# Kernel tuning notes

Hardware: AMD Instinct MI355X
Metric: run time of the kernel (lower is better)

Reference implementation:

```python
import jax, jax.numpy as jnp
import numpy as np
from jax import lax

BETA = 0.1

def setup_inputs() -> dict:
    key = jax.random.key(0)
    k = jax.random.split(key, 6)
    B, T, H, V = 2, 1024, 1024, 64000
    return {
        "_input": jax.random.normal(k[0], (B, T, H), jnp.float32) * 0.02,
        "weight": jax.random.normal(k[1], (V, H), jnp.float32) * 0.02,
        "attention_mask": (jax.random.uniform(k[2], (B, T)) < 0.9).astype(jnp.float32),
        "rewards": jax.random.normal(k[3], (B,), jnp.float32),
        "ref_input": jax.random.normal(k[4], (B, T, H), jnp.float32) * 0.02,
        "ref_weight": jax.random.normal(k[5], (V, H), jnp.float32) * 0.02,
    }


def _grpo(log_probs, attention_mask, rewards, ref_log_probs, beta):
    # log_probs: [B,T,V]
    chosen = jnp.argmax(log_probs, axis=-1)  # [B,T] int
    tok_lp = jnp.take_along_axis(log_probs, chosen[..., None], axis=-1)[..., 0]  # [B,T]
    ref_tok_lp = lax.stop_gradient(
        jnp.take_along_axis(ref_log_probs, chosen[..., None], axis=-1)[..., 0]
    )
    adv = (rewards - rewards.mean()) / (jnp.std(rewards, ddof=1) + 1e-8)  # [B]
    ratio = jnp.exp(tok_lp - lax.stop_gradient(tok_lp))  # == 1 in fwd, grad-carrying
    policy_loss = -ratio * adv[:, None]
    d = ref_tok_lp - tok_lp
    kl = jnp.exp(d) - d - 1.0
    per_tok = (policy_loss + beta * kl) * attention_mask
    seqlen = jnp.clip(attention_mask.sum(axis=1), 1.0)
    loss = (per_tok.sum(axis=1) / seqlen).mean()
    metrics = (
        tok_lp.mean(),
        jnp.std(tok_lp, ddof=1),
        log_probs.mean(),
        (kl * attention_mask).sum(axis=1).mean() / attention_mask.sum(axis=1).mean(),
    )
    return loss, metrics


def reference(_input, weight, attention_mask, rewards, ref_input, ref_weight):
    logits = jnp.einsum("bth,vh->btv", _input, weight)
    log_probs = jax.nn.log_softmax(logits, axis=-1)
    ref_logits = jnp.einsum("bth,vh->btv", ref_input, ref_weight)
    ref_log_probs = lax.stop_gradient(jax.nn.log_softmax(ref_logits, axis=-1))
    loss, metrics = _grpo(log_probs, attention_mask, rewards, ref_log_probs, BETA)
    return (loss, *metrics)
```

## Files before the change

### kernel.cpp

```cpp
#include <hip/hip_runtime.h>
#include <math.h>

#define GRPO_BETA 0.1f

constexpr int BM = 128;
constexpr int BN = 256;
constexpr int BK = 32;

typedef __attribute__((ext_vector_type(4))) float   f32x4;
typedef __attribute__((ext_vector_type(8))) __bf16  bf16x8;

__device__ __forceinline__ float sexp_fast(float a) { return __expf(fminf(a, 0.f)); }
__device__ __forceinline__ float sexp(float a)      { return expf(fminf(a, 0.f)); }

__device__ __forceinline__ bf16x8 cvt8(float4 a, float4 b) {
  bf16x8 r;
  r[0] = (__bf16)a.x; r[1] = (__bf16)a.y; r[2] = (__bf16)a.z; r[3] = (__bf16)a.w;
  r[4] = (__bf16)b.x; r[5] = (__bf16)b.y; r[6] = (__bf16)b.z; r[7] = (__bf16)b.w;
  return r;
}

__device__ __forceinline__ void bar_lgkm() {
  asm volatile("s_waitcnt lgkmcnt(0)\n\ts_barrier" ::: "memory");
}

__global__ __launch_bounds__(256)
void cvt_bf16_kernel(const float* __restrict__ src, __bf16* __restrict__ dst,
                     long long n8)
{
  long long i = (long long)blockIdx.x * blockDim.x + threadIdx.x;
  const long long stride = (long long)gridDim.x * blockDim.x;
  for (; i < n8; i += stride) {
    const float4 a = *reinterpret_cast<const float4*>(src + i * 8);
    const float4 b = *reinterpret_cast<const float4*>(src + i * 8 + 4);
    *reinterpret_cast<bf16x8*>(dst + i * 8) = cvt8(a, b);
  }
}

template <bool CVT, bool FULL>
__global__ __launch_bounds__(512, 4)
void fused_gemm_reduce(const float* __restrict__ AfP, const float* __restrict__ WfP,
                       const float* __restrict__ AfR, const float* __restrict__ WfR,
                       const __bf16* __restrict__ AhP, const __bf16* __restrict__ WhP,
                       const __bf16* __restrict__ AhR, const __bf16* __restrict__ WhR,
                       float* __restrict__ partP, float* __restrict__ partR,
                       int M, int K, int V, int NC, int NL, int gx)
{
  __shared__ __align__(16) unsigned short lds_a[BM * 64];
  __shared__ __align__(16) unsigned short lds_w[BN * 64];
  __shared__ __align__(16) float4 lds_red[BM * 4];

  const int tid  = threadIdx.x;
  const int lane = tid & 63;
  const int wave = tid >> 6;
  const int wm   = wave >> 2;
  const int wn   = wave & 3;
  const int l15  = lane & 15;
  const int q    = lane >> 4;

  const int nb  = gridDim.x;
  int wl = blockIdx.x;
  if ((nb & 7) == 0) wl = (wl & 7) * (nb >> 3) + (wl >> 3);
  const bool isPol = (wl & 1) == 0;
  const int  w2    = wl >> 1;
  const int  bx    = w2 % gx;
  const int  chunk = w2 / gx;
  const int  row0  = bx * BM;

  const float*  Af = isPol ? AfP : AfR;
  const float*  Wf = isPol ? WfP : WfR;
  const __bf16* Ah = isPol ? AhP : AhR;
  const __bf16* Wh = isPol ? WhP : WhR;

  const int t3 = tid & 3;
  const int r4 = tid >> 2;
  const int stw = ((t3 * 16) ^ ((r4 & 7) << 4));
  const int sta = r4 * 128 + stw;

  const int arow = min(row0 + r4, M - 1);
  const int aro  = arow * K + t3 * 8;

  const int swzr  = ((q * 16) ^ ((l15 & 7) << 4));
  const int aoff0 = (wm * 64 + l15) * 128 + swzr;
  const int woff0 = (wn * 64 + l15) * 128 + swzr;

  float rm = -INFINITY, rse = 0.f, rsum = 0.f;
  int   ridx = 0x7fffffff;

  const int NS = K / BK;

  for (int sub = 0; sub < NL; ++sub) {
    const int v0 = (chunk * NL + sub) * BN;
    if (v0 >= V) break;

    int wro[2];
#pragma unroll
    for (int i = 0; i < 2; ++i)
      wro[i] = min(v0 + r4 + 128 * i, V - 1) * K + t3 * 8;

    f32x4 acc[4][4];
#pragma unroll
    for (int i = 0; i < 4; ++i)
#pragma unroll
      for (int j = 0; j < 4; ++j) acc[i][j] = (f32x4){0.f, 0.f, 0.f, 0.f};

    float4 aF[2], wF[2][2];
    bf16x8 aH, wH[2];

    if constexpr (CVT) {
      aF[0] = *reinterpret_cast<const float4*>(Af + aro);
      aF[1] = *reinterpret_cast<const float4*>(Af + aro + 4);
#pragma unroll
      for (int i = 0; i < 2; ++i) {
        wF[i][0] = *reinterpret_cast<const float4*>(Wf + wro[i]);
        wF[i][1] = *reinterpret_cast<const float4*>(Wf + wro[i] + 4);
      }
      *reinterpret_cast<bf16x8*>(reinterpret_cast<char*>(lds_a) + sta) = cvt8(aF[0], aF[1]);
#pragma unroll
      for (int i = 0; i < 2; ++i)
        *reinterpret_cast<bf16x8*>(reinterpret_cast<char*>(lds_w) + (r4 + 128 * i) * 128 + stw) =
            cvt8(wF[i][0], wF[i][1]);
      if (NS > 1) {
        aF[0] = *reinterpret_cast<const float4*>(Af + aro + BK);
        aF[1] = *reinterpret_cast<const float4*>(Af + aro + BK + 4);
#pragma unroll
        for (int i = 0; i < 2; ++i) {
          wF[i][0] = *reinterpret_cast<const float4*>(Wf + wro[i] + BK);
          wF[i][1] = *reinterpret_cast<const float4*>(Wf + wro[i] + BK + 4);
        }
      }
    } else {
      aH = *reinterpret_cast<const bf16x8*>(Ah + aro);
#pragma unroll
      for (int i = 0; i < 2; ++i)
        wH[i] = *reinterpret_cast<const bf16x8*>(Wh + wro[i]);
      *reinterpret_cast<bf16x8*>(reinterpret_cast<char*>(lds_a) + sta) = aH;
#pragma unroll
      for (int i = 0; i < 2; ++i)
        *reinterpret_cast<bf16x8*>(reinterpret_cast<char*>(lds_w) + (r4 + 128 * i) * 128 + stw) = wH[i];
      if (NS > 1) {
        aH = *reinterpret_cast<const bf16x8*>(Ah + aro + BK);
#pragma unroll
        for (int i = 0; i < 2; ++i)
          wH[i] = *reinterpret_cast<const bf16x8*>(Wh + wro[i] + BK);
      }
    }
    bar_lgkm();

    for (int s = 0; s < NS; ++s) {
      const int p = (s & 1) << 6;

      bf16x8 afr[4];
#pragma unroll
      for (int f = 0; f < 4; ++f)
        afr[f] = *reinterpret_cast<const bf16x8*>(
            reinterpret_cast<const char*>(lds_a) + (aoff0 ^ p) + f * 2048);
      __builtin_amdgcn_s_setprio(1);
#pragma unroll
      for (int fn = 0; fn < 4; ++fn) {
        bf16x8 wfr = *reinterpret_cast<const bf16x8*>(
            reinterpret_cast<const char*>(lds_w) + (woff0 ^ p) + fn * 2048);
#pragma unroll
        for (int fm = 0; fm < 4; ++fm)
          acc[fm][fn] = __builtin_amdgcn_mfma_f32_16x16x32_bf16(
              afr[fm], wfr, acc[fm][fn], 0, 0, 0);
      }
      __builtin_amdgcn_s_setprio(0);

      if (s + 1 < NS) {
        const int p1 = ((s + 1) & 1) << 6;
        if constexpr (CVT) {
          *reinterpret_cast<bf16x8*>(reinterpret_cast<char*>(lds_a) + (sta ^ p1)) =
              cvt8(aF[0], aF[1]);
#pragma unroll
          for (int i = 0; i < 2; ++i)
            *reinterpret_cast<bf16x8*>(
                reinterpret_cast<char*>(lds_w) + (((r4 + 128 * i) * 128 + stw) ^ p1)) =
                cvt8(wF[i][0], wF[i][1]);
          if (s + 2 < NS) {
            const int kf = (s + 2) * BK;
            aF[0] = *reinterpret_cast<const float4*>(Af + aro + kf);
            aF[1] = *reinterpret_cast<const float4*>(Af + aro + kf + 4);
#pragma unroll
            for (int i = 0; i < 2; ++i) {
              wF[i][0] = *reinterpret_cast<const float4*>(Wf + wro[i] + kf);
              wF[i][1] = *reinterpret_cast<const float4*>(Wf + wro[i] + kf + 4);
            }
          }
        } else {
          *reinterpret_cast<bf16x8*>(reinterpret_cast<char*>(lds_a) + (sta ^ p1)) = aH;
#pragma unroll
          for (int i = 0; i < 2; ++i)
            *reinterpret_cast<bf16x8*>(
                reinterpret_cast<char*>(lds_w) + (((r4 + 128 * i) * 128 + stw) ^ p1)) = wH[i];
          if (s + 2 < NS) {
            const int kf = (s + 2) * BK;
            aH = *reinterpret_cast<const bf16x8*>(Ah + aro + kf);
#pragma unroll
            for (int i = 0; i < 2; ++i)
              wH[i] = *reinterpret_cast<const bf16x8*>(Wh + wro[i] + kf);
          }
        }
      }
      bar_lgkm();
    }

#pragma unroll
    for (int fm = 0; fm < 4; ++fm) {
#pragma unroll
      for (int reg = 0; reg < 4; ++reg) {
        float lm = -INFINITY;
#pragma unroll
        for (int fn = 0; fn < 4; ++fn) {
          if (FULL || v0 + wn * 64 + fn * 16 + l15 < V)
            lm = fmaxf(lm, acc[fm][fn][reg]);
        }
#pragma unroll
        for (int d = 1; d < 16; d <<= 1) lm = fmaxf(lm, __shfl_xor(lm, d));
        float se = 0.f, sm = 0.f; int li = 0x7fffffff;
#pragma unroll
        for (int fn = 0; fn < 4; ++fn) {
          const int v = v0 + wn * 64 + fn * 16 + l15;
          if (FULL || v < V) {
            const float x = acc[fm][fn][reg];
            se += __expf(x - lm);
            if (isPol) {
              sm += x;
              if (x == lm) li = min(li, v);
            }
          }
        }
        if (isPol) {
#pragma unroll
          for (int d = 1; d < 16; d <<= 1) {
            se += __shfl_xor(se, d);
            sm += __shfl_xor(sm, d);
            li  = min(li, __shfl_xor(li, d));
          }
        } else {
#pragma unroll
          for (int d = 1; d < 16; d <<= 1) se += __shfl_xor(se, d);
        }
        if (l15 == 0) {
          const int row = wm * 64 + fm * 16 + q * 4 + reg;
          lds_red[row * 4 + wn] = make_float4(lm, se, sm, __int_as_float(li));
        }
      }
    }
    __syncthreads();

    if (tid < BM) {
      float4 p0 = lds_red[tid * 4];
      float m = p0.x, se = p0.y, sm = p0.z; int idx = __float_as_int(p0.w);
#pragma unroll
      for (int j = 1; j < 4; ++j) {
        const float4 t = lds_red[tid * 4 + j];
        const int ti = __float_as_int(t.w);
        const float nm = fmaxf(m, t.x);
        se = se * sexp_fast(m - nm) + t.y * sexp_fast(t.x - nm);
        if (isPol) {
          sm += t.z;
          if (t.x > m || (t.x == m && ti < idx)) idx = ti;
        }
        m = nm;
      }
      const float nm = fmaxf(rm, m);
      rse = rse * sexp_fast(rm - nm) + se * sexp_fast(m - nm);
      if (isPol) {
        rsum += sm;
        if (m > rm || (m == rm && idx < ridx)) ridx = idx;
      }
      rm = nm;
    }
    __syncthreads();
  }

  if (tid < BM) {
    const int row = row0 + tid;
    if (row < M) {
      if (isPol) {
        reinterpret_cast<float4*>(partP)[(size_t)row * NC + chunk] =
            make_float4(rm, rse, rsum, __int_as_float(ridx));
      } else {
        reinterpret_cast<float2*>(partR)[(size_t)row * NC + chunk] =
            make_float2(rm, rse);
      }
    }
  }
}

__global__ __launch_bounds__(256)
void combine_kernel(const float4* __restrict__ partP,
                    const float2* __restrict__ partR,
                    const float* __restrict__ refA,
                    const float* __restrict__ refW,
                    float4* __restrict__ rowtab,
                    int M, int K, int V, int NC)
{
  const int row = blockIdx.x;
  const int tid = threadIdx.x;

  __shared__ float redf[256];
  __shared__ int   redi[256];
  __shared__ float s_M, s_SE, s_SUM, s_Mr, s_SEr, s_dot;
  __shared__ int   s_idx;

  float m = -INFINITY, se = 0.f, sm = 0.f; int idx = 0x7fffffff;
  for (int i = tid; i < NC; i += 256) {
    float4 p = partP[(size_t)row * NC + i];
    int pi = __float_as_int(p.w);
    float nm = fmaxf(m, p.x);
    se = se * sexp(m - nm) + p.y * sexp(p.x - nm);
    if (p.x > m || (p.x == m && pi < idx)) idx = pi;
    m = nm;
    sm += p.z;
  }
  redf[tid] = m; redi[tid] = idx;
  __syncthreads();
  for (int s = 128; s > 0; s >>= 1) {
    if (tid < s) {
      float om = redf[tid + s]; int oi = redi[tid + s];
      if (om > redf[tid] || (om == redf[tid] && oi < redi[tid])) { redf[tid] = om; redi[tid] = oi; }
    }
    __syncthreads();
  }
  if (tid == 0) { s_M = redf[0]; s_idx = redi[0]; }
  __syncthreads();
  const float Mp = s_M; const int chosen = s_idx;

  float contrib = se * sexp(m - Mp);
  __syncthreads();
  redf[tid] = contrib; __syncthreads();
  for (int s = 128; s > 0; s >>= 1) { if (tid < s) redf[tid] += redf[tid + s]; __syncthreads(); }
  if (tid == 0) s_SE = redf[0];
  __syncthreads();
  redf[tid] = sm; __syncthreads();
  for (int s = 128; s > 0; s >>= 1) { if (tid < s) redf[tid] += redf[tid + s]; __syncthreads(); }
  if (tid == 0) s_SUM = redf[0];
  __syncthreads();

  float mr = -INFINITY, ser = 0.f;
  for (int i = tid; i < NC; i += 256) {
    float2 p = partR[(size_t)row * NC + i];
    float nm = fmaxf(mr, p.x);
    ser = ser * sexp(mr - nm) + p.y * sexp(p.x - nm);
    mr = nm;
  }
  redf[tid] = mr; __syncthreads();
  for (int s = 128; s > 0; s >>= 1) { if (tid < s) redf[tid] = fmaxf(redf[tid], redf[tid + s]); __syncthreads(); }
  if (tid == 0) s_Mr = redf[0];
  __syncthreads();
  const float Mr = s_Mr;
  float contribr = ser * sexp(mr - Mr);
  __syncthreads();
  redf[tid] = contribr; __syncthreads();
  for (int s = 128; s > 0; s >>= 1) { if (tid < s) redf[tid] += redf[tid + s]; __syncthreads(); }
  if (tid == 0) s_SEr = redf[0];
  __syncthreads();

  float dp = 0.f;
  const float* ar = refA + (size_t)row * K;
  const float* wr = refW + (size_t)chosen * K;
  for (int j = tid * 4; j < K; j += 256 * 4) {
    float4 x = *reinterpret_cast<const float4*>(ar + j);
    float4 y = *reinterpret_cast<const float4*>(wr + j);
    dp = fmaf(x.x, y.x, dp);
    dp = fmaf(x.y, y.y, dp);
    dp = fmaf(x.z, y.z, dp);
    dp = fmaf(x.w, y.w, dp);
  }
  __syncthreads();
  redf[tid] = dp; __syncthreads();
  for (int s = 128; s > 0; s >>= 1) { if (tid < s) redf[tid] += redf[tid + s]; __syncthreads(); }
  if (tid == 0) s_dot = redf[0];
  __syncthreads();

  if (tid == 0) {
    float lse     = Mp + logf(s_SE);
    float tok     = Mp - lse;
    float ref_lse = Mr + logf(s_SEr);
    float ref_tok = s_dot - ref_lse;
    float d  = ref_tok - tok;
    float kl = expm1f(d) - d;
    float rm3 = s_SUM / (float)V - lse;
    rowtab[row] = make_float4(tok, kl, rm3, 0.f);
  }
}

__global__ __launch_bounds__(256)
void final_kernel(const float4* __restrict__ rowtab,
                  const float* __restrict__ mask,
                  const float* __restrict__ rewards,
                  float* __restrict__ out,
                  int M, int B, int T)
{
  const int tid = threadIdx.x;
  __shared__ float redf[256];
  __shared__ float s_mean, s_m3, s_var;
  __shared__ float s_kl[16], s_cnt[16];

  float st = 0.f, sm3 = 0.f;
  for (int r = tid; r < M; r += 256) {
    float4 v = rowtab[r];
    st += v.x; sm3 += v.z;
  }
  redf[tid] = st; __syncthreads();
  for (int s = 128; s > 0; s >>= 1) { if (tid < s) redf[tid] += redf[tid + s]; __syncthreads(); }
  if (tid == 0) s_mean = redf[0] / (float)M;
  __syncthreads();
  redf[tid] = sm3; __syncthreads();
  for (int s = 128; s > 0; s >>= 1) { if (tid < s) redf[tid] += redf[tid + s]; __syncthreads(); }
  if (tid == 0) s_m3 = redf[0] / (float)M;
  __syncthreads();

  const float mean = s_mean;
  float sv = 0.f;
  for (int r = tid; r < M; r += 256) { float d = rowtab[r].x - mean; sv = fmaf(d, d, sv); }
  __syncthreads();
  redf[tid] = sv; __syncthreads();
  for (int s = 128; s > 0; s >>= 1) { if (tid < s) redf[tid] += redf[tid + s]; __syncthreads(); }
  if (tid == 0) s_var = redf[0];
  __syncthreads();

  const int nb = B < 16 ? B : 16;
  for (int b = 0; b < nb; ++b) {
    float lk = 0.f, lc = 0.f;
    for (int t = tid; t < T; t += 256) {
      int r = b * T + t;
      float mk = mask[r];
      lk = fmaf(rowtab[r].y, mk, lk);
      lc += mk;
    }
    __syncthreads();
    redf[tid] = lk; __syncthreads();
    for (int s = 128; s > 0; s >>= 1) { if (tid < s) redf[tid] += redf[tid + s]; __syncthreads(); }
    if (tid == 0) s_kl[b] = redf[0];
    __syncthreads();
    redf[tid] = lc; __syncthreads();
    for (int s = 128; s > 0; s >>= 1) { if (tid < s) redf[tid] += redf[tid + s]; __syncthreads(); }
    if (tid == 0) s_cnt[b] = redf[0];
    __syncthreads();
  }

  if (tid == 0) {
    float rmean = 0.f;
    for (int b = 0; b < B; ++b) rmean += rewards[b];
    rmean /= (float)B;
    float rv = 0.f;
    for (int b = 0; b < B; ++b) { float d = rewards[b] - rmean; rv += d * d; }
    float rstd = sqrtf(rv / (float)(B > 1 ? B - 1 : 1));

    float loss = 0.f, m4n = 0.f, m4d = 0.f;
    for (int b = 0; b < nb; ++b) {
      float adv  = (rewards[b] - rmean) / (rstd + 1e-8f);
      float cnt  = s_cnt[b];
      float seql = fmaxf(cnt, 1.0f);
      loss += (-adv * cnt + GRPO_BETA * s_kl[b]) / seql;
      m4n += s_kl[b];
      m4d += cnt;
    }
    loss /= (float)B;

    out[0] = loss;
    out[1] = s_mean;
    out[2] = sqrtf(s_var / (float)(M - 1));
    out[3] = s_m3;
    out[4] = m4n / m4d;
  }
}

extern "C" void kernel_launch(void* const* d_in, const int* in_sizes, int n_in,
                              void* d_out, int out_size, void* d_ws, size_t ws_size,
                              hipStream_t stream)
{
  if (n_in < 6) return;
  const float* A       = (const float*)d_in[0];
  const float* W       = (const float*)d_in[1];
  const float* mask    = (const float*)d_in[2];
  const float* rewards = (const float*)d_in[3];
  const float* rA      = (const float*)d_in[4];
  const float* rW      = (const float*)d_in[5];

  const int M = in_sizes[2];
  const int B = in_sizes[3];
  const int T = M / B;
  const int K = in_sizes[0] / M;
  const int V = in_sizes[1] / K;

  const int gx = (M + BM - 1) / BM;
  const bool full = (V % BN) == 0;

  const size_t aBytes = (size_t)M * K * sizeof(__bf16);
  const size_t wBytes = (size_t)V * K * sizeof(__bf16);
  auto partBytes = [&](int nl) -> size_t {
    int nc = (V + BN * nl - 1) / (BN * nl);
    return (size_t)M * nc * 16 + (size_t)M * nc * 8 + (size_t)M * 16;
  };

  int NL = 1;
  bool canPrep = false;
  if (K % 8 == 0) {
    for (int nl = 1; nl <= 1024; nl <<= 1) {
      size_t pb = (partBytes(nl) + 255) & ~(size_t)255;
      if (pb + 2 * aBytes + 2 * wBytes <= ws_size) { NL = nl; canPrep = true; break; }
    }
  }
  if (!canPrep) {
    NL = 1;
    while (partBytes(NL) > ws_size && NL < 1024) NL <<= 1;
  }
  const int NC = (V + BN * NL - 1) / (BN * NL);

  float* partP  = (float*)d_ws;
  float* partR  = partP + (size_t)M * NC * 4;
  float* rowtab = partR + (size_t)M * NC * 2;

  dim3 g1(2 * gx * NC), b1(512);

  if (canPrep) {
    size_t pb = (partBytes(NL) + 255) & ~(size_t)255;
    __bf16* Ab  = (__bf16*)((char*)d_ws + pb);
    __bf16* rAb = Ab  + (size_t)M * K;
    __bf16* Wb  = rAb + (size_t)M * K;
    __bf16* rWb = Wb  + (size_t)V * K;

    const long long nA8 = (long long)M * K / 8;
    const long long nW8 = (long long)V * K / 8;
    cvt_bf16_kernel<<<dim3(512),  dim3(256), 0, stream>>>(A,  Ab,  nA8);
    cvt_bf16_kernel<<<dim3(512),  dim3(256), 0, stream>>>(rA, rAb, nA8);
    cvt_bf16_kernel<<<dim3(2048), dim3(256), 0, stream>>>(W,  Wb,  nW8);
    cvt_bf16_kernel<<<dim3(2048), dim3(256), 0, stream>>>(rW, rWb, nW8);

    if (full) {
      fused_gemm_reduce<false, true ><<<g1, b1, 0, stream>>>(
          nullptr, nullptr, nullptr, nullptr, Ab, Wb, rAb, rWb,
          partP, partR, M, K, V, NC, NL, gx);
    } else {
      fused_gemm_reduce<false, false><<<g1, b1, 0, stream>>>(
          nullptr, nullptr, nullptr, nullptr, Ab, Wb, rAb, rWb,
          partP, partR, M, K, V, NC, NL, gx);
    }
  } else {
    if (full) {
      fused_gemm_reduce<true , true ><<<g1, b1, 0, stream>>>(
          A, W, rA, rW, nullptr, nullptr, nullptr, nullptr,
          partP, partR, M, K, V, NC, NL, gx);
    } else {
      fused_gemm_reduce<true , false><<<g1, b1, 0, stream>>>(
          A, W, rA, rW, nullptr, nullptr, nullptr, nullptr,
          partP, partR, M, K, V, NC, NL, gx);
    }
  }

  combine_kernel<<<dim3(M), dim3(256), 0, stream>>>(
      (const float4*)partP, (const float2*)partR, rA, rW, (float4*)rowtab, M, K, V, NC);
  final_kernel<<<dim3(1), dim3(256), 0, stream>>>(
      (const float4*)rowtab, mask, rewards, (float*)d_out, M, B, T);
}
```

Baseline: 878.7 us.

## Load A fragments directly from global into registers, bypassing LDS

The A-tile shared-memory buffer is removed. Each wave now loads its own MFMA A fragments straight from global memory into registers, using a register double buffer (A/B sets) across a manually unrolled pair of K-steps, while W continues to go through double-buffered LDS. This drops the LDS writes and reads for A and shrinks shared memory per block. The costs are redundant global loads of A across the four wn waves, higher register pressure that may hurt the 4-blocks-per-CU occupancy, and less coalesced fragment-shaped global access.

```diff
diff --git a/kernel.cpp b/kernel.cpp
--- a/kernel.cpp
+++ b/kernel.cpp
@@ -46,7 +46,6 @@
                        float* __restrict__ partP, float* __restrict__ partR,
                        int M, int K, int V, int NC, int NL, int gx)
 {
-  __shared__ __align__(16) unsigned short lds_a[BM * 64];
   __shared__ __align__(16) unsigned short lds_w[BN * 64];
   __shared__ __align__(16) float4 lds_red[BM * 4];
 
@@ -75,13 +74,13 @@
   const int t3 = tid & 3;
   const int r4 = tid >> 2;
   const int stw = ((t3 * 16) ^ ((r4 & 7) << 4));
-  const int sta = r4 * 128 + stw;
-
-  const int arow = min(row0 + r4, M - 1);
-  const int aro  = arow * K + t3 * 8;
+
+  int afo[4];
+#pragma unroll
+  for (int f = 0; f < 4; ++f)
+    afo[f] = min(row0 + wm * 64 + f * 16 + l15, M - 1) * K + q * 8;
 
   const int swzr  = ((q * 16) ^ ((l15 & 7) << 4));
-  const int aoff0 = (wm * 64 + l15) * 128 + swzr;
   const int woff0 = (wn * 64 + l15) * 128 + swzr;
 
   float rm = -INFINITY, rse = 0.f, rsum = 0.f;
@@ -104,25 +103,25 @@
 #pragma unroll
       for (int j = 0; j < 4; ++j) acc[i][j] = (f32x4){0.f, 0.f, 0.f, 0.f};
 
-    float4 aF[2], wF[2][2];
-    bf16x8 aH, wH[2];
+    bf16x8 wH[2];
+    float4 wF[2][2];
+    bf16x8 afA[4], afB[4];
+    float4 afFA[4][2], afFB[4][2];
 
     if constexpr (CVT) {
-      aF[0] = *reinterpret_cast<const float4*>(Af + aro);
-      aF[1] = *reinterpret_cast<const float4*>(Af + aro + 4);
 #pragma unroll
       for (int i = 0; i < 2; ++i) {
-        wF[i][0] = *reinterpret_cast<const float4*>(Wf + wro[i]);
-        wF[i][1] = *reinterpret_cast<const float4*>(Wf + wro[i] + 4);
-      }
-      *reinterpret_cast<bf16x8*>(reinterpret_cast<char*>(lds_a) + sta) = cvt8(aF[0], aF[1]);
-#pragma unroll
-      for (int i = 0; i < 2; ++i)
+        const float4 w0 = *reinterpret_cast<const float4*>(Wf + wro[i]);
+        const float4 w1 = *reinterpret_cast<const float4*>(Wf + wro[i] + 4);
         *reinterpret_cast<bf16x8*>(reinterpret_cast<char*>(lds_w) + (r4 + 128 * i) * 128 + stw) =
-            cvt8(wF[i][0], wF[i][1]);
+            cvt8(w0, w1);
+      }
+#pragma unroll
+      for (int f = 0; f < 4; ++f) {
+        afFA[f][0] = *reinterpret_cast<const float4*>(Af + afo[f]);
+        afFA[f][1] = *reinterpret_cast<const float4*>(Af + afo[f] + 4);
+      }
       if (NS > 1) {
-        aF[0] = *reinterpret_cast<const float4*>(Af + aro + BK);
-        aF[1] = *reinterpret_cast<const float4*>(Af + aro + BK + 4);
 #pragma unroll
         for (int i = 0; i < 2; ++i) {
           wF[i][0] = *reinterpret_cast<const float4*>(Wf + wro[i] + BK);
@@ -130,16 +129,14 @@
         }
       }
     } else {
-      aH = *reinterpret_cast<const bf16x8*>(Ah + aro);
 #pragma unroll
       for (int i = 0; i < 2; ++i)
-        wH[i] = *reinterpret_cast<const bf16x8*>(Wh + wro[i]);
-      *reinterpret_cast<bf16x8*>(reinterpret_cast<char*>(lds_a) + sta) = aH;
-#pragma unroll
-      for (int i = 0; i < 2; ++i)
-        *reinterpret_cast<bf16x8*>(reinterpret_cast<char*>(lds_w) + (r4 + 128 * i) * 128 + stw) = wH[i];
+        *reinterpret_cast<bf16x8*>(reinterpret_cast<char*>(lds_w) + (r4 + 128 * i) * 128 + stw) =
+            *reinterpret_cast<const bf16x8*>(Wh + wro[i]);
+#pragma unroll
+      for (int f = 0; f < 4; ++f)
+        afA[f] = *reinterpret_cast<const bf16x8*>(Ah + afo[f]);
       if (NS > 1) {
-        aH = *reinterpret_cast<const bf16x8*>(Ah + aro + BK);
 #pragma unroll
         for (int i = 0; i < 2; ++i)
           wH[i] = *reinterpret_cast<const bf16x8*>(Wh + wro[i] + BK);
@@ -147,40 +144,49 @@
     }
     bar_lgkm();
 
-    for (int s = 0; s < NS; ++s) {
-      const int p = (s & 1) << 6;
-
-      bf16x8 afr[4];
-#pragma unroll
-      for (int f = 0; f < 4; ++f)
-        afr[f] = *reinterpret_cast<const bf16x8*>(
-            reinterpret_cast<const char*>(lds_a) + (aoff0 ^ p) + f * 2048);
-      __builtin_amdgcn_s_setprio(1);
-#pragma unroll
-      for (int fn = 0; fn < 4; ++fn) {
-        bf16x8 wfr = *reinterpret_cast<const bf16x8*>(
-            reinterpret_cast<const char*>(lds_w) + (woff0 ^ p) + fn * 2048);
-#pragma unroll
-        for (int fm = 0; fm < 4; ++fm)
-          acc[fm][fn] = __builtin_amdgcn_mfma_f32_16x16x32_bf16(
-              afr[fm], wfr, acc[fm][fn], 0, 0, 0);
-      }
-      __builtin_amdgcn_s_setprio(0);
-
+    for (int s = 0; s < NS; s += 2) {
       if (s + 1 < NS) {
-        const int p1 = ((s + 1) & 1) << 6;
+        const int kf = (s + 1) * BK;
         if constexpr (CVT) {
-          *reinterpret_cast<bf16x8*>(reinterpret_cast<char*>(lds_a) + (sta ^ p1)) =
-              cvt8(aF[0], aF[1]);
+#pragma unroll
+          for (int f = 0; f < 4; ++f) {
+            afFB[f][0] = *reinterpret_cast<const float4*>(Af + afo[f] + kf);
+            afFB[f][1] = *reinterpret_cast<const float4*>(Af + afo[f] + kf + 4);
+          }
+        } else {
+#pragma unroll
+          for (int f = 0; f < 4; ++f)
+            afB[f] = *reinterpret_cast<const bf16x8*>(Ah + afo[f] + kf);
+        }
+      }
+      {
+        bf16x8 av[4];
+#pragma unroll
+        for (int f = 0; f < 4; ++f) {
+          if constexpr (CVT) av[f] = cvt8(afFA[f][0], afFA[f][1]);
+          else               av[f] = afA[f];
+        }
+        __builtin_amdgcn_s_setprio(1);
+#pragma unroll
+        for (int fn = 0; fn < 4; ++fn) {
+          bf16x8 wfr = *reinterpret_cast<const bf16x8*>(
+              reinterpret_cast<const char*>(lds_w) + woff0 + fn * 2048);
+#pragma unroll
+          for (int fm = 0; fm < 4; ++fm)
+            acc[fm][fn] = __builtin_amdgcn_mfma_f32_16x16x32_bf16(
+                av[fm], wfr, acc[fm][fn], 0, 0, 0);
+        }
+        __builtin_amdgcn_s_setprio(0);
+      }
+      if (s + 1 < NS) {
+        if constexpr (CVT) {
 #pragma unroll
           for (int i = 0; i < 2; ++i)
             *reinterpret_cast<bf16x8*>(
-                reinterpret_cast<char*>(lds_w) + (((r4 + 128 * i) * 128 + stw) ^ p1)) =
+                reinterpret_cast<char*>(lds_w) + (((r4 + 128 * i) * 128 + stw) ^ 64)) =
                 cvt8(wF[i][0], wF[i][1]);
           if (s + 2 < NS) {
             const int kf = (s + 2) * BK;
-            aF[0] = *reinterpret_cast<const float4*>(Af + aro + kf);
-            aF[1] = *reinterpret_cast<const float4*>(Af + aro + kf + 4);
 #pragma unroll
             for (int i = 0; i < 2; ++i) {
               wF[i][0] = *reinterpret_cast<const float4*>(Wf + wro[i] + kf);
@@ -188,14 +194,12 @@
             }
           }
         } else {
-          *reinterpret_cast<bf16x8*>(reinterpret_cast<char*>(lds_a) + (sta ^ p1)) = aH;
 #pragma unroll
           for (int i = 0; i < 2; ++i)
             *reinterpret_cast<bf16x8*>(
-                reinterpret_cast<char*>(lds_w) + (((r4 + 128 * i) * 128 + stw) ^ p1)) = wH[i];
+                reinterpret_cast<char*>(lds_w) + (((r4 + 128 * i) * 128 + stw) ^ 64)) = wH[i];
           if (s + 2 < NS) {
             const int kf = (s + 2) * BK;
-            aH = *reinterpret_cast<const bf16x8*>(Ah + aro + kf);
 #pragma unroll
             for (int i = 0; i < 2; ++i)
               wH[i] = *reinterpret_cast<const bf16x8*>(Wh + wro[i] + kf);
@@ -203,6 +207,71 @@
         }
       }
       bar_lgkm();
+
+      if (s + 1 < NS) {
+        if (s + 2 < NS) {
+          const int kf = (s + 2) * BK;
+          if constexpr (CVT) {
+#pragma unroll
+            for (int f = 0; f < 4; ++f) {
+              afFA[f][0] = *reinterpret_cast<const float4*>(Af + afo[f] + kf);
+              afFA[f][1] = *reinterpret_cast<const float4*>(Af + afo[f] + kf + 4);
+            }
+          } else {
+#pragma unroll
+            for (int f = 0; f < 4; ++f)
+              afA[f] = *reinterpret_cast<const bf16x8*>(Ah + afo[f] + kf);
+          }
+        }
+        {
+          bf16x8 av[4];
+#pragma unroll
+          for (int f = 0; f < 4; ++f) {
+            if constexpr (CVT) av[f] = cvt8(afFB[f][0], afFB[f][1]);
+            else               av[f] = afB[f];
+          }
+          __builtin_amdgcn_s_setprio(1);
+#pragma unroll
+          for (int fn = 0; fn < 4; ++fn) {
+            bf16x8 wfr = *reinterpret_cast<const bf16x8*>(
+                reinterpret_cast<const char*>(lds_w) + (woff0 ^ 64) + fn * 2048);
+#pragma unroll
+            for (int fm = 0; fm < 4; ++fm)
+              acc[fm][fn] = __builtin_amdgcn_mfma_f32_16x16x32_bf16(
+                  av[fm], wfr, acc[fm][fn], 0, 0, 0);
+          }
+          __builtin_amdgcn_s_setprio(0);
+        }
+        if (s + 2 < NS) {
+          if constexpr (CVT) {
+#pragma unroll
+            for (int i = 0; i < 2; ++i)
+              *reinterpret_cast<bf16x8*>(
+                  reinterpret_cast<char*>(lds_w) + (r4 + 128 * i) * 128 + stw) =
+                  cvt8(wF[i][0], wF[i][1]);
+            if (s + 3 < NS) {
+              const int kf = (s + 3) * BK;
+#pragma unroll
+              for (int i = 0; i < 2; ++i) {
+                wF[i][0] = *reinterpret_cast<const float4*>(Wf + wro[i] + kf);
+                wF[i][1] = *reinterpret_cast<const float4*>(Wf + wro[i] + kf + 4);
+              }
+            }
+          } else {
+#pragma unroll
+            for (int i = 0; i < 2; ++i)
+              *reinterpret_cast<bf16x8*>(
+                  reinterpret_cast<char*>(lds_w) + (r4 + 128 * i) * 128 + stw) = wH[i];
+            if (s + 3 < NS) {
+              const int kf = (s + 3) * BK;
+#pragma unroll
+              for (int i = 0; i < 2; ++i)
+                wH[i] = *reinterpret_cast<const bf16x8*>(Wh + wro[i] + kf);
+            }
+          }
+        }
+        bar_lgkm();
+      }
     }
 
 #pragma unroll
```

Result: slower. 1.379 ms (+56.9%).

## Use direct global-to-LDS loads with BK=64 tiles in bf16 GEMM path

Applied to the files above, without the earlier changes.

Replaces the register-staged, double-buffered bf16 tile loading in the non-converting GEMM path with global_load_lds direct-to-LDS transfers. Each iteration covers 64 K-elements, stored with an XOR-swizzled source column so the existing swizzled fragment reads still line up. This removes VGPR staging and ds_write instructions, but it drops the overlap between the next tile's loads and the current MFMAs and adds two barriers per K-step. The prep path now requires K%64.

```diff
diff --git a/kernel.cpp b/kernel.cpp
--- a/kernel.cpp
+++ b/kernel.cpp
@@ -5,7 +5,6 @@
 
 constexpr int BM = 128;
 constexpr int BN = 256;
-constexpr int BK = 32;
 
 typedef __attribute__((ext_vector_type(4))) float   f32x4;
 typedef __attribute__((ext_vector_type(8))) __bf16  bf16x8;
@@ -22,6 +21,12 @@
 
 __device__ __forceinline__ void bar_lgkm() {
   asm volatile("s_waitcnt lgkmcnt(0)\n\ts_barrier" ::: "memory");
+}
+
+__device__ __forceinline__ void gload_lds16(const void* g, void* l) {
+  __builtin_amdgcn_global_load_lds(
+      (const __attribute__((address_space(1))) void*)g,
+      (__attribute__((address_space(3))) void*)l, 16, 0, 0);
 }
 
 __global__ __launch_bounds__(256)
@@ -72,13 +77,14 @@
   const __bf16* Ah = isPol ? AhP : AhR;
   const __bf16* Wh = isPol ? WhP : WhR;
 
+  const int rsub = lane >> 3;
+  const int srcg = ((lane & 7) ^ rsub) * 8;
+
   const int t3 = tid & 3;
   const int r4 = tid >> 2;
   const int stw = ((t3 * 16) ^ ((r4 & 7) << 4));
   const int sta = r4 * 128 + stw;
-
-  const int arow = min(row0 + r4, M - 1);
-  const int aro  = arow * K + t3 * 8;
+  const int aroF = min(row0 + r4, M - 1) * K + t3 * 8;
 
   const int swzr  = ((q * 16) ^ ((l15 & 7) << 4));
   const int aoff0 = (wm * 64 + l15) * 128 + swzr;
@@ -87,29 +93,74 @@
   float rm = -INFINITY, rse = 0.f, rsum = 0.f;
   int   ridx = 0x7fffffff;
 
-  const int NS = K / BK;
-
   for (int sub = 0; sub < NL; ++sub) {
     const int v0 = (chunk * NL + sub) * BN;
     if (v0 >= V) break;
 
-    int wro[2];
-#pragma unroll
-    for (int i = 0; i < 2; ++i)
-      wro[i] = min(v0 + r4 + 128 * i, V - 1) * K + t3 * 8;
-
     f32x4 acc[4][4];
 #pragma unroll
     for (int i = 0; i < 4; ++i)
 #pragma unroll
       for (int j = 0; j < 4; ++j) acc[i][j] = (f32x4){0.f, 0.f, 0.f, 0.f};
 
-    float4 aF[2], wF[2][2];
-    bf16x8 aH, wH[2];
-
-    if constexpr (CVT) {
-      aF[0] = *reinterpret_cast<const float4*>(Af + aro);
-      aF[1] = *reinterpret_cast<const float4*>(Af + aro + 4);
+    if constexpr (!CVT) {
+      const __bf16* asrc[2];
+#pragma unroll
+      for (int c = 0; c < 2; ++c) {
+        const int r = (wave + c * 8) * 8 + rsub;
+        asrc[c] = Ah + (size_t)min(row0 + r, M - 1) * K + srcg;
+      }
+      const __bf16* wsrc[4];
+#pragma unroll
+      for (int c = 0; c < 4; ++c) {
+        const int r = (wave + c * 8) * 8 + rsub;
+        wsrc[c] = Wh + (size_t)min(v0 + r, V - 1) * K + srcg;
+      }
+
+      for (int kt = 0; kt < K; kt += 64) {
+        __syncthreads();
+#pragma unroll
+        for (int c = 0; c < 2; ++c)
+          gload_lds16(asrc[c] + kt,
+                      reinterpret_cast<char*>(lds_a) + (wave + c * 8) * 1024);
+#pragma unroll
+        for (int c = 0; c < 4; ++c)
+          gload_lds16(wsrc[c] + kt,
+                      reinterpret_cast<char*>(lds_w) + (wave + c * 8) * 1024);
+        __syncthreads();
+
+#pragma unroll
+        for (int kh = 0; kh < 2; ++kh) {
+          const int p = kh << 6;
+          bf16x8 afr[4];
+#pragma unroll
+          for (int f = 0; f < 4; ++f)
+            afr[f] = *reinterpret_cast<const bf16x8*>(
+                reinterpret_cast<const char*>(lds_a) + (aoff0 ^ p) + f * 2048);
+          __builtin_amdgcn_s_setprio(1);
+#pragma unroll
+          for (int fn = 0; fn < 4; ++fn) {
+            bf16x8 wfr = *reinterpret_cast<const bf16x8*>(
+                reinterpret_cast<const char*>(lds_w) + (woff0 ^ p) + fn * 2048);
+#pragma unroll
+            for (int fm = 0; fm < 4; ++fm)
+              acc[fm][fn] = __builtin_amdgcn_mfma_f32_16x16x32_bf16(
+                  afr[fm], wfr, acc[fm][fn], 0, 0, 0);
+          }
+          __builtin_amdgcn_s_setprio(0);
+        }
+      }
+      __syncthreads();
+    } else {
+      const int NS = K / 32;
+      int wro[2];
+#pragma unroll
+      for (int i = 0; i < 2; ++i)
+        wro[i] = min(v0 + r4 + 128 * i, V - 1) * K + t3 * 8;
+
+      float4 aF[2], wF[2][2];
+      aF[0] = *reinterpret_cast<const float4*>(Af + aroF);
+      aF[1] = *reinterpret_cast<const float4*>(Af + aroF + 4);
 #pragma unroll
       for (int i = 0; i < 2; ++i) {
         wF[i][0] = *reinterpret_cast<const float4*>(Wf + wro[i]);
@@ -121,55 +172,37 @@
         *reinterpret_cast<bf16x8*>(reinterpret_cast<char*>(lds_w) + (r4 + 128 * i) * 128 + stw) =
             cvt8(wF[i][0], wF[i][1]);
       if (NS > 1) {
-        aF[0] = *reinterpret_cast<const float4*>(Af + aro + BK);
-        aF[1] = *reinterpret_cast<const float4*>(Af + aro + BK + 4);
+        aF[0] = *reinterpret_cast<const float4*>(Af + aroF + 32);
+        aF[1] = *reinterpret_cast<const float4*>(Af + aroF + 32 + 4);
 #pragma unroll
         for (int i = 0; i < 2; ++i) {
-          wF[i][0] = *reinterpret_cast<const float4*>(Wf + wro[i] + BK);
-          wF[i][1] = *reinterpret_cast<const float4*>(Wf + wro[i] + BK + 4);
-        }
-      }
-    } else {
-      aH = *reinterpret_cast<const bf16x8*>(Ah + aro);
-#pragma unroll
-      for (int i = 0; i < 2; ++i)
-        wH[i] = *reinterpret_cast<const bf16x8*>(Wh + wro[i]);
-      *reinterpret_cast<bf16x8*>(reinterpret_cast<char*>(lds_a) + sta) = aH;
-#pragma unroll
-      for (int i = 0; i < 2; ++i)
-        *reinterpret_cast<bf16x8*>(reinterpret_cast<char*>(lds_w) + (r4 + 128 * i) * 128 + stw) = wH[i];
-      if (NS > 1) {
-        aH = *reinterpret_cast<const bf16x8*>(Ah + aro + BK);
-#pragma unroll
-        for (int i = 0; i < 2; ++i)
-          wH[i] = *reinterpret_cast<const bf16x8*>(Wh + wro[i] + BK);
-      }
-    }
-    bar_lgkm();
-
-    for (int s = 0; s < NS; ++s) {
-      const int p = (s & 1) << 6;
-
-      bf16x8 afr[4];
-#pragma unroll
-      for (int f = 0; f < 4; ++f)
-        afr[f] = *reinterpret_cast<const bf16x8*>(
-            reinterpret_cast<const char*>(lds_a) + (aoff0 ^ p) + f * 2048);
-      __builtin_amdgcn_s_setprio(1);
-#pragma unroll
-      for (int fn = 0; fn < 4; ++fn) {
-        bf16x8 wfr = *reinterpret_cast<const bf16x8*>(
-            reinterpret_cast<const char*>(lds_w) + (woff0 ^ p) + fn * 2048);
-#pragma unroll
-        for (int fm = 0; fm < 4; ++fm)
-          acc[fm][fn] = __builtin_amdgcn_mfma_f32_16x16x32_bf16(
-              afr[fm], wfr, acc[fm][fn], 0, 0, 0);
-      }
-      __builtin_amdgcn_s_setprio(0);
-
-      if (s + 1 < NS) {
-        const int p1 = ((s + 1) & 1) << 6;
-        if constexpr (CVT) {
+          wF[i][0] = *reinterpret_cast<const float4*>(Wf + wro[i] + 32);
+          wF[i][1] = *reinterpret_cast<const float4*>(Wf + wro[i] + 32 + 4);
+        }
+      }
+      bar_lgkm();
+
+      for (int s = 0; s < NS; ++s) {
+        const int p = (s & 1) << 6;
+        bf16x8 afr[4];
+#pragma unroll
+        for (int f = 0; f < 4; ++f)
+          afr[f] = *reinterpret_cast<const bf16x8*>(
+              reinterpret_cast<const char*>(lds_a) + (aoff0 ^ p) + f * 2048);
+        __builtin_amdgcn_s_setprio(1);
+#pragma unroll
+        for (int fn = 0; fn < 4; ++fn) {
+          bf16x8 wfr = *reinterpret_cast<const bf16x8*>(
+              reinterpret_cast<const char*>(lds_w) + (woff0 ^ p) + fn * 2048);
+#pragma unroll
+          for (int fm = 0; fm < 4; ++fm)
+            acc[fm][fn] = __builtin_amdgcn_mfma_f32_16x16x32_bf16(
+                afr[fm], wfr, acc[fm][fn], 0, 0, 0);
+        }
+        __builtin_amdgcn_s_setprio(0);
+
+        if (s + 1 < NS) {
+          const int p1 = ((s + 1) & 1) << 6;
           *reinterpret_cast<bf16x8*>(reinterpret_cast<char*>(lds_a) + (sta ^ p1)) =
               cvt8(aF[0], aF[1]);
 #pragma unroll
@@ -178,31 +211,18 @@
                 reinterpret_cast<char*>(lds_w) + (((r4 + 128 * i) * 128 + stw) ^ p1)) =
                 cvt8(wF[i][0], wF[i][1]);
           if (s + 2 < NS) {
-            const int kf = (s + 2) * BK;
-            aF[0] = *reinterpret_cast<const float4*>(Af + aro + kf);
-            aF[1] = *reinterpret_cast<const float4*>(Af + aro + kf + 4);
+            const int kf = (s + 2) * 32;
+            aF[0] = *reinterpret_cast<const float4*>(Af + aroF + kf);
+            aF[1] = *reinterpret_cast<const float4*>(Af + aroF + kf + 4);
 #pragma unroll
             for (int i = 0; i < 2; ++i) {
               wF[i][0] = *reinterpret_cast<const float4*>(Wf + wro[i] + kf);
               wF[i][1] = *reinterpret_cast<const float4*>(Wf + wro[i] + kf + 4);
             }
           }
-        } else {
-          *reinterpret_cast<bf16x8*>(reinterpret_cast<char*>(lds_a) + (sta ^ p1)) = aH;
-#pragma unroll
-          for (int i = 0; i < 2; ++i)
-            *reinterpret_cast<bf16x8*>(
-                reinterpret_cast<char*>(lds_w) + (((r4 + 128 * i) * 128 + stw) ^ p1)) = wH[i];
-          if (s + 2 < NS) {
-            const int kf = (s + 2) * BK;
-            aH = *reinterpret_cast<const bf16x8*>(Ah + aro + kf);
-#pragma unroll
-            for (int i = 0; i < 2; ++i)
-              wH[i] = *reinterpret_cast<const bf16x8*>(Wh + wro[i] + kf);
-          }
-        }
-      }
-      bar_lgkm();
+        }
+        bar_lgkm();
+      }
     }
 
 #pragma unroll
@@ -499,7 +519,7 @@
 
   int NL = 1;
   bool canPrep = false;
-  if (K % 8 == 0) {
+  if (K % 64 == 0) {
     for (int nl = 1; nl <= 1024; nl <<= 1) {
       size_t pb = (partBytes(nl) + 255) & ~(size_t)255;
       if (pb + 2 * aBytes + 2 * wBytes <= ws_size) { NL = nl; canPrep = true; break; }
```

New measurement: 877.8 us. Within noise of the previous version (-0.1%).
